# Kernel tuning notes

Hardware: AMD Instinct MI355X
Metric: run time of the kernel (lower is better)

## Reference

```python
import jax, jax.numpy as jnp
import numpy as np

N_NODES = 50000
N_EDGES = 500000
N_GRAPHS = 256
D_IN, D_H1, D_H2, D_H3, D_OUT = 768, 256, 128, 64, 2


def _glorot(key, shape):
    fan_in, fan_out = shape[1], shape[0]
    lim = float(np.sqrt(6.0 / (fan_in + fan_out)))
    return jax.random.uniform(key, shape, jnp.float32, -lim, lim)


def setup_inputs() -> dict:
    key = jax.random.key(0)
    ks = jax.random.split(key, 12)
    x = jax.random.normal(ks[0], (N_NODES, D_IN), jnp.float32)
    edge_index = jax.random.randint(ks[1], (2, N_EDGES), 0, N_NODES, jnp.int64)
    batch = jnp.sort(jax.random.randint(ks[2], (N_NODES,), 0, N_GRAPHS, jnp.int64))
    return {
        "x": x,
        "edge_index": edge_index,
        "batch": batch,
        # SAGEConv1: out = lin_l(mean_aggr) + lin_r(x); bias only on lin_l (PyG default)
        "W1_l": _glorot(ks[3], (D_H1, D_IN)),
        "b1_l": jnp.zeros((D_H1,), jnp.float32),
        "W1_r": _glorot(ks[4], (D_H1, D_IN)),
        # SAGEConv2
        "W2_l": _glorot(ks[5], (D_H2, D_H1)),
        "b2_l": jnp.zeros((D_H2,), jnp.float32),
        "W2_r": _glorot(ks[6], (D_H2, D_H1)),
        # MLP head
        "W3": _glorot(ks[7], (D_H3, D_H2)),
        "b3": jnp.zeros((D_H3,), jnp.float32),
        "W4": _glorot(ks[8], (D_OUT, D_H3)),
        "b4": jnp.zeros((D_OUT,), jnp.float32),
    }


def _sage_conv(x, src, dst, deg_inv, W_l, b_l, W_r):
    # mean aggregation of neighbor features: scatter-add then divide by in-degree
    aggr = jax.ops.segment_sum(x[src], dst, num_segments=N_NODES)  # [N, d]
    aggr = aggr * deg_inv[:, None]
    return aggr @ W_l.T + b_l + x @ W_r.T


def reference(x, edge_index, batch, W1_l, b1_l, W1_r, W2_l, b2_l, W2_r, W3, b3, W4, b4):
    src, dst = edge_index[0], edge_index[1]
    deg = jax.ops.segment_sum(jnp.ones((N_EDGES,), x.dtype), dst, num_segments=N_NODES)
    deg_inv = jnp.where(deg > 0, 1.0 / jnp.maximum(deg, 1.0), 0.0)

    h = jax.nn.relu(_sage_conv(x, src, dst, deg_inv, W1_l, b1_l, W1_r))
    h = jax.nn.relu(_sage_conv(h, src, dst, deg_inv, W2_l, b2_l, W2_r))

    # global_mean_pool over graph ids
    pooled = jax.ops.segment_sum(h, batch, num_segments=N_GRAPHS)  # [G, 128]
    cnt = jax.ops.segment_sum(jnp.ones((N_NODES,), h.dtype), batch, num_segments=N_GRAPHS)
    pooled = pooled / jnp.maximum(cnt, 1.0)[:, None]

    # dropout is identity in eval mode
    h = pooled @ W3.T + b3
    h = h @ W4.T + b4
    return jax.nn.softmax(h, axis=-1)
```

## Files before the change

### kernel.cpp

```cpp
#include <hip/hip_runtime.h>
#include <cstdint>
#include <cstddef>

#define N_NODES 50000
#define N_EDGES 500000
#define N_GRAPHS 256
#define D_IN 768
#define D_H1 256
#define D_H2 128

typedef __attribute__((ext_vector_type(8))) __bf16 bf16x8;
typedef __attribute__((ext_vector_type(4))) float f32x4;

__device__ __forceinline__ float bf2f(uint32_t u) {
    union { uint32_t i; float f; } v; v.i = u << 16; return v.f;
}
__device__ __forceinline__ uint32_t f2bf(float f) {
    union { float f; uint32_t i; } v; v.f = f;
    uint32_t u = v.i;
    return (u + 0x7FFFu + ((u >> 16) & 1u)) >> 16;
}

#define HIST4_BLKS 489
#define PACKA4_BLKS 4688
#define PACKW1_BLKS 192
#define PACKW2_BLKS 32
#define NCHUNK_A 4800000
__global__ __launch_bounds__(256) void k_pack_hist(
    const float* __restrict__ x, uint16_t* __restrict__ xp,
    const float* __restrict__ W1l, const float* __restrict__ W1r, uint16_t* __restrict__ W1p,
    const float* __restrict__ W2l, const float* __restrict__ W2r, uint16_t* __restrict__ W2p,
    const int* __restrict__ e_dst, int* __restrict__ deg)
{
    int b = blockIdx.x, t = threadIdx.x;
    if (b < HIST4_BLKS) {
        int base = b * 1024 + t;
        #pragma unroll
        for (int j = 0; j < 4; ++j) {
            int e = base + j * 256;
            if (e < N_EDGES) atomicAdd(&deg[e_dst[e]], 1);
        }
    } else if (b < HIST4_BLKS + PACKA4_BLKS) {
        int c0 = (b - HIST4_BLKS) * 1024 + t;
        float4 u[4], v[4];
        #pragma unroll
        for (int j = 0; j < 4; ++j) {
            int c = c0 + j * 256; if (c > NCHUNK_A - 1) c = NCHUNK_A - 1;
            int l = c & 63, tt = c >> 6;
            int kt = tt % 24, mt = tt / 24;
            const float* p = x + (size_t)(mt * 16 + (l & 15)) * 768 + kt * 32 + (l >> 4) * 8;
            u[j] = *(const float4*)p;
            v[j] = *(const float4*)(p + 4);
        }
        #pragma unroll
        for (int j = 0; j < 4; ++j) {
            int c = c0 + j * 256; if (c > NCHUNK_A - 1) c = NCHUNK_A - 1;
            uint4 o;
            o.x = f2bf(u[j].x) | (f2bf(u[j].y) << 16);
            o.y = f2bf(u[j].z) | (f2bf(u[j].w) << 16);
            o.z = f2bf(v[j].x) | (f2bf(v[j].y) << 16);
            o.w = f2bf(v[j].z) | (f2bf(v[j].w) << 16);
            *(uint4*)(xp + (size_t)c * 8) = o;
        }
    } else if (b < HIST4_BLKS + PACKA4_BLKS + PACKW1_BLKS) {
        int c = (b - HIST4_BLKS - PACKA4_BLKS) * 256 + t;
        int l = c & 63, tt = c >> 6;
        int kt = tt % 24, mt = tt / 24;
        int row = mt * 16 + (l & 15);
        const float* src = (row < 256) ? (W1l + (size_t)row * 768)
                                       : (W1r + (size_t)(row - 256) * 768);
        const float* p = src + kt * 32 + (l >> 4) * 8;
        float4 u = *(const float4*)p, v = *(const float4*)(p + 4);
        uint4 o;
        o.x = f2bf(u.x) | (f2bf(u.y) << 16);
        o.y = f2bf(u.z) | (f2bf(u.w) << 16);
        o.z = f2bf(v.x) | (f2bf(v.y) << 16);
        o.w = f2bf(v.z) | (f2bf(v.w) << 16);
        *(uint4*)(W1p + (size_t)c * 8) = o;
    } else {
        int c = (b - HIST4_BLKS - PACKA4_BLKS - PACKW1_BLKS) * 256 + t;
        int l = c & 63, tt = c >> 6;
        int kt = tt % 8, mt = tt / 8;
        int row = mt * 16 + (l & 15);
        const float* src = (row < 128) ? (W2l + (size_t)row * 256)
                                       : (W2r + (size_t)(row - 128) * 256);
        const float* p = src + kt * 32 + (l >> 4) * 8;
        float4 u = *(const float4*)p, v = *(const float4*)(p + 4);
        uint4 o;
        o.x = f2bf(u.x) | (f2bf(u.y) << 16);
        o.y = f2bf(u.z) | (f2bf(u.w) << 16);
        o.z = f2bf(v.x) | (f2bf(v.y) << 16);
        o.w = f2bf(v.z) | (f2bf(v.w) << 16);
        *(uint4*)(W2p + (size_t)c * 8) = o;
    }
}

__global__ __launch_bounds__(256) void k_scan(
    const int* __restrict__ deg, int* __restrict__ row_start, int* __restrict__ cursor,
    float* __restrict__ deg_inv, int* __restrict__ bsum, int n, int nb)
{
    __shared__ int buf[256];
    __shared__ int bbuf[256];
    int t = threadIdx.x, b = blockIdx.x, i = b * 256 + t;
    int v = (i < n) ? deg[i] : 0;
    buf[t] = v; __syncthreads();
    for (int off = 1; off < 256; off <<= 1) {
        int u = (t >= off) ? buf[t - off] : 0;
        __syncthreads(); buf[t] += u; __syncthreads();
    }
    if (t == 255) atomicExch(&bsum[b], buf[255] + 1);
    int w = 0;
    if (t < nb) {
        do { w = atomicAdd(&bsum[t], 0); } while (w == 0);
        w -= 1;
    }
    bbuf[t] = w; __syncthreads();
    for (int off = 1; off < 256; off <<= 1) {
        int u = (t >= off) ? bbuf[t - off] : 0;
        __syncthreads(); bbuf[t] += u; __syncthreads();
    }
    int base = (b > 0) ? bbuf[b - 1] : 0;
    if (i < n) {
        int rs = base + buf[t] - v;
        row_start[i] = rs;
        cursor[i] = rs;
        deg_inv[i] = (v > 0) ? (1.0f / (float)v) : 0.0f;
    }
    if (b == 0 && t == 0) row_start[n] = N_EDGES;
}

#define NSLAB 782
#define G1_GROUPS 98
#define G1_BLKS (G1_GROUPS * 16)
#define FILL_BLKS 1954
__global__ __launch_bounds__(256, 2) void k_gemm1_fill(
    const uint16_t* __restrict__ Ap, const uint16_t* __restrict__ Bp,
    uint16_t* __restrict__ Cl, uint16_t* __restrict__ Cr,
    const int* __restrict__ e_src, const int* __restrict__ e_dst,
    int* __restrict__ cursor, int* __restrict__ csr_src)
{
    int t = threadIdx.x;
    if (blockIdx.x >= G1_BLKS) {
        int e = (blockIdx.x - G1_BLKS) * 256 + t;
        if (e < N_EDGES) {
            int d = e_dst[e];
            int pos = atomicAdd(&cursor[d], 1);
            csr_src[pos] = e_src[e];
        }
        return;
    }
    const int i = blockIdx.x;
    const int pr = (i >> 4) * 8 + (i & 7);
    const int half = (i >> 3) & 1;
    if (pr >= NSLAB) return;
    const int KT = 24;
    const int wave = t >> 6, lane = t & 63;
    const int fr = lane & 15, fq = lane >> 4;
    const int bm = pr * 64;
    const int mtiles = (N_NODES + 15) >> 4;

    const bf16x8* ap[4];
    const bf16x8* bp[4];
    #pragma unroll
    for (int mi = 0; mi < 4; ++mi) {
        int mt = (bm >> 4) + mi;
        if (mt > mtiles - 1) mt = mtiles - 1;
        ap[mi] = (const bf16x8*)Ap + (size_t)mt * KT * 64 + lane;
    }
    #pragma unroll
    for (int ni = 0; ni < 4; ++ni) {
        int nt = half * 16 + wave * 4 + ni;
        bp[ni] = (const bf16x8*)Bp + (size_t)nt * KT * 64 + lane;
    }

    f32x4 acc[4][4] = {};
    bf16x8 a0[4], b0[4], a1[4], b1[4];

    auto lA = [&](int kt, bf16x8* d) {
        #pragma unroll
        for (int mi = 0; mi < 4; ++mi) d[mi] = ap[mi][kt * 64];
    };
    auto lB = [&](int kt, bf16x8* d) {
        #pragma unroll
        for (int ni = 0; ni < 4; ++ni) d[ni] = bp[ni][kt * 64];
    };
    auto step = [&](bf16x8* a, bf16x8* b) {
        #pragma unroll
        for (int mi = 0; mi < 4; ++mi)
            #pragma unroll
            for (int ni = 0; ni < 4; ++ni)
                acc[mi][ni] = __builtin_amdgcn_mfma_f32_16x16x32_bf16(
                    a[mi], b[ni], acc[mi][ni], 0, 0, 0);
    };

    lA(0, a0); lB(0, b0);
    for (int ks = 0; ks < KT; ks += 2) {
        lA(ks + 1, a1); lB(ks + 1, b1);
        step(a0, b0);
        if (ks + 2 < KT) { lA(ks + 2, a0); lB(ks + 2, b0); }
        step(a1, b1);
    }

    uint16_t* __restrict__ C = half ? Cr : Cl;
    #pragma unroll
    for (int mi = 0; mi < 4; ++mi) {
        #pragma unroll
        for (int r = 0; r < 4; ++r) {
            int row = bm + mi * 16 + fq * 4 + r;
            if (row >= N_NODES) continue;
            #pragma unroll
            for (int ni = 0; ni < 4; ++ni) {
                int col = wave * 64 + ni * 16 + fr;
                C[(size_t)row * 256 + col] = (uint16_t)f2bf(acc[mi][ni][r]);
            }
        }
    }
}

__global__ __launch_bounds__(256, 2) void k_mgemm(
    const uint16_t* __restrict__ Ap, const uint16_t* __restrict__ Bp,
    uint16_t* __restrict__ C, int M, int N, int KT)
{
    const int tid = threadIdx.x;
    const int wave = tid >> 6, lane = tid & 63;
    const int fr = lane & 15, fq = lane >> 4;
    const int bn = blockIdx.x * 256, bm = blockIdx.y * 128;
    const int wm = (wave >> 1) * 64, wn = (wave & 1) * 128;
    const int mtiles = (M + 15) >> 4;

    const bf16x8* ap[4];
    const bf16x8* bp[8];
    #pragma unroll
    for (int mi = 0; mi < 4; ++mi) {
        int mt = ((bm + wm) >> 4) + mi;
        if (mt > mtiles - 1) mt = mtiles - 1;
        ap[mi] = (const bf16x8*)Ap + (size_t)mt * KT * 64 + lane;
    }
    #pragma unroll
    for (int ni = 0; ni < 8; ++ni) {
        int nt = ((bn + wn) >> 4) + ni;
        bp[ni] = (const bf16x8*)Bp + (size_t)nt * KT * 64 + lane;
    }

    f32x4 acc[4][8] = {};
    bf16x8 a0[4], b0[8], a1[4], b1[8];

    auto lA = [&](int kt, bf16x8* d) {
        #pragma unroll
        for (int mi = 0; mi < 4; ++mi) d[mi] = ap[mi][kt * 64];
    };
    auto lB = [&](int kt, bf16x8* d) {
        #pragma unroll
        for (int ni = 0; ni < 8; ++ni) d[ni] = bp[ni][kt * 64];
    };
    auto step = [&](bf16x8* a, bf16x8* b) {
        #pragma unroll
        for (int mi = 0; mi < 4; ++mi)
            #pragma unroll
            for (int ni = 0; ni < 8; ++ni)
                acc[mi][ni] = __builtin_amdgcn_mfma_f32_16x16x32_bf16(
                    a[mi], b[ni], acc[mi][ni], 0, 0, 0);
    };

    lA(0, a0); lB(0, b0);
    for (int ks = 0; ks < KT; ks += 2) {
        lA(ks + 1, a1); lB(ks + 1, b1);
        step(a0, b0);
        if (ks + 2 < KT) { lA(ks + 2, a0); lB(ks + 2, b0); }
        step(a1, b1);
    }

    #pragma unroll
    for (int mi = 0; mi < 4; ++mi) {
        #pragma unroll
        for (int r = 0; r < 4; ++r) {
            int row = bm + wm + mi * 16 + fq * 4 + r;
            if (row >= M) continue;
            #pragma unroll
            for (int ni = 0; ni < 8; ++ni) {
                int col = bn + wn + ni * 16 + fr;
                C[(size_t)row * N + col] = (uint16_t)f2bf(acc[mi][ni][r]);
            }
        }
    }
}

__global__ __launch_bounds__(256) void k_agg1(
    const uint16_t* __restrict__ yl, const uint16_t* __restrict__ yr,
    const int* __restrict__ row_start, const int* __restrict__ csr,
    const float* __restrict__ deg_inv, const float* __restrict__ bias,
    uint16_t* __restrict__ h1p)
{
    int node = blockIdx.x * 8 + (threadIdx.x >> 5);
    if (node >= N_NODES) return;
    int c = threadIdx.x & 31;
    int s = row_start[node], e = row_start[node + 1];
    float a[8] = {};
    int p = s;
    auto accum = [&](uint4 t0) {
        a[0] += bf2f(t0.x & 0xFFFF); a[1] += bf2f(t0.x >> 16);
        a[2] += bf2f(t0.y & 0xFFFF); a[3] += bf2f(t0.y >> 16);
        a[4] += bf2f(t0.z & 0xFFFF); a[5] += bf2f(t0.z >> 16);
        a[6] += bf2f(t0.w & 0xFFFF); a[7] += bf2f(t0.w >> 16);
    };
    for (; p + 3 < e; p += 4) {
        uint4 t0 = *(const uint4*)(yl + (size_t)csr[p]     * 256 + c * 8);
        uint4 t1 = *(const uint4*)(yl + (size_t)csr[p + 1] * 256 + c * 8);
        uint4 t2 = *(const uint4*)(yl + (size_t)csr[p + 2] * 256 + c * 8);
        uint4 t3 = *(const uint4*)(yl + (size_t)csr[p + 3] * 256 + c * 8);
        accum(t0); accum(t1); accum(t2); accum(t3);
    }
    for (; p < e; ++p)
        accum(*(const uint4*)(yl + (size_t)csr[p] * 256 + c * 8));
    float w = deg_inv[node];
    uint4 tx = *(const uint4*)(yr + (size_t)node * 256 + c * 8);
    float4 b0 = *(const float4*)(bias + c * 8);
    float4 b1 = *(const float4*)(bias + c * 8 + 4);
    float v0 = fmaxf(a[0] * w + bf2f(tx.x & 0xFFFF) + b0.x, 0.f);
    float v1 = fmaxf(a[1] * w + bf2f(tx.x >> 16)    + b0.y, 0.f);
    float v2 = fmaxf(a[2] * w + bf2f(tx.y & 0xFFFF) + b0.z, 0.f);
    float v3 = fmaxf(a[3] * w + bf2f(tx.y >> 16)    + b0.w, 0.f);
    float v4 = fmaxf(a[4] * w + bf2f(tx.z & 0xFFFF) + b1.x, 0.f);
    float v5 = fmaxf(a[5] * w + bf2f(tx.z >> 16)    + b1.y, 0.f);
    float v6 = fmaxf(a[6] * w + bf2f(tx.w & 0xFFFF) + b1.z, 0.f);
    float v7 = fmaxf(a[7] * w + bf2f(tx.w >> 16)    + b1.w, 0.f);
    uint4 o;
    o.x = f2bf(v0) | (f2bf(v1) << 16);
    o.y = f2bf(v2) | (f2bf(v3) << 16);
    o.z = f2bf(v4) | (f2bf(v5) << 16);
    o.w = f2bf(v6) | (f2bf(v7) << 16);
    uint32_t addr = (((node >> 4) * 8 + (c >> 2)) * 64 + (c & 3) * 16 + (node & 15));
    *(uint4*)(h1p + (size_t)addr * 8) = o;
}

__global__ __launch_bounds__(256) void k_agg2(
    const uint16_t* __restrict__ y, const int* __restrict__ row_start,
    const int* __restrict__ csr, const float* __restrict__ deg_inv,
    const float* __restrict__ bias, float* __restrict__ out)
{
    int node = blockIdx.x * 4 + (threadIdx.x >> 6);
    if (node >= N_NODES) return;
    int lane = threadIdx.x & 63;
    int s = row_start[node], e = row_start[node + 1];
    float a0 = 0.f, a1 = 0.f;
    int p = s;
    for (; p + 3 < e; p += 4) {
        uint32_t t0 = *(const uint32_t*)(y + (size_t)csr[p]     * 256 + lane * 2);
        uint32_t t1 = *(const uint32_t*)(y + (size_t)csr[p + 1] * 256 + lane * 2);
        uint32_t t2 = *(const uint32_t*)(y + (size_t)csr[p + 2] * 256 + lane * 2);
        uint32_t t3 = *(const uint32_t*)(y + (size_t)csr[p + 3] * 256 + lane * 2);
        a0 += bf2f(t0 & 0xFFFF) + bf2f(t1 & 0xFFFF) + bf2f(t2 & 0xFFFF) + bf2f(t3 & 0xFFFF);
        a1 += bf2f(t0 >> 16)    + bf2f(t1 >> 16)    + bf2f(t2 >> 16)    + bf2f(t3 >> 16);
    }
    for (; p < e; ++p) {
        uint32_t t0 = *(const uint32_t*)(y + (size_t)csr[p] * 256 + lane * 2);
        a0 += bf2f(t0 & 0xFFFF);
        a1 += bf2f(t0 >> 16);
    }
    float w = deg_inv[node];
    uint32_t tx = *(const uint32_t*)(y + (size_t)node * 256 + 128 + lane * 2);
    float2 b = *(const float2*)(bias + lane * 2);
    float2 o;
    o.x = fmaxf(a0 * w + bf2f(tx & 0xFFFF) + b.x, 0.f);
    o.y = fmaxf(a1 * w + bf2f(tx >> 16)    + b.y, 0.f);
    *(float2*)(out + (size_t)node * 128 + lane * 2) = o;
}

__global__ void k_poolhead(const float* __restrict__ h2, const int* __restrict__ batch,
                           const float* __restrict__ W3, const float* __restrict__ b3,
                           const float* __restrict__ W4, const float* __restrict__ b4,
                           float* __restrict__ out)
{
    int g = blockIdx.x;
    __shared__ int s_lo, s_hi;
    __shared__ float p[128];
    __shared__ float hid[64];
    __shared__ float logit[2];
    int t = threadIdx.x;
    if (t == 0) {
        int lo = 0, hi = N_NODES;
        while (lo < hi) { int m = (lo + hi) >> 1; if (batch[m] < g) lo = m + 1; else hi = m; }
        s_lo = lo;
        int lo2 = lo, hi2 = N_NODES;
        while (lo2 < hi2) { int m = (lo2 + hi2) >> 1; if (batch[m] < g + 1) lo2 = m + 1; else hi2 = m; }
        s_hi = lo2;
    }
    __syncthreads();
    float sum = 0.f;
    for (int i = s_lo; i < s_hi; ++i) sum += h2[(size_t)i * D_H2 + t];
    int cnt = s_hi - s_lo;
    p[t] = sum / (float)(cnt > 0 ? cnt : 1);
    __syncthreads();
    if (t < 64) {
        float s = b3[t];
        #pragma unroll 4
        for (int k = 0; k < 128; ++k) s = fmaf(p[k], W3[t * 128 + k], s);
        hid[t] = s;
    }
    __syncthreads();
    if (t < 2) {
        float l = b4[t];
        for (int k = 0; k < 64; ++k) l = fmaf(hid[k], W4[t * 64 + k], l);
        logit[t] = l;
    }
    __syncthreads();
    if (t == 0) {
        float m = fmaxf(logit[0], logit[1]);
        float e0 = expf(logit[0] - m), e1 = expf(logit[1] - m);
        float inv = 1.0f / (e0 + e1);
        out[g * 2 + 0] = e0 * inv;
        out[g * 2 + 1] = e1 * inv;
    }
}

extern "C" void kernel_launch(void* const* d_in, const int* in_sizes, int n_in,
                              void* d_out, int out_size, void* d_ws, size_t ws_size,
                              hipStream_t stream)
{
    const float* x     = (const float*)d_in[0];
    const int*   ei    = (const int*)d_in[1];
    const int*   batch = (const int*)d_in[2];
    const float* W1l   = (const float*)d_in[3];
    const float* b1l   = (const float*)d_in[4];
    const float* W1r   = (const float*)d_in[5];
    const float* W2l   = (const float*)d_in[6];
    const float* b2l   = (const float*)d_in[7];
    const float* W2r   = (const float*)d_in[8];
    const float* W3    = (const float*)d_in[9];
    const float* b3    = (const float*)d_in[10];
    const float* W4    = (const float*)d_in[11];
    const float* b4    = (const float*)d_in[12];
    float* out = (float*)d_out;

    const int* e_src = ei;
    const int* e_dst = ei + N_EDGES;

    char* ws = (char*)d_ws;
    size_t off = 0;
    auto alloc = [&](size_t bytes) -> void* {
        void* p = ws + off;
        off = (off + bytes + 255) & ~(size_t)255;
        return p;
    };
    int*      deg       = (int*)alloc((size_t)(N_NODES + 256) * 4);
    int*      bsum      = deg + N_NODES;
    int*      row_start = (int*)alloc((size_t)(N_NODES + 1) * 4);
    int*      cursor    = (int*)alloc((size_t)N_NODES * 4);
    int*      csr_src   = (int*)alloc((size_t)N_EDGES * 4);
    float*    deg_inv   = (float*)alloc((size_t)N_NODES * 4);
    uint16_t* W1p       = (uint16_t*)alloc((size_t)512 * 768 * 2);
    uint16_t* W2p       = (uint16_t*)alloc((size_t)256 * 256 * 2);
    uint16_t* xp        = (uint16_t*)alloc((size_t)N_NODES * D_IN * 2);
    uint16_t* y1        = (uint16_t*)alloc((size_t)N_NODES * 512 * 2);
    uint16_t* h1p       = (uint16_t*)alloc((size_t)N_NODES * 256 * 2);

    uint16_t* y1l = y1;
    uint16_t* y1r = y1 + (size_t)N_NODES * 256;
    uint16_t* y2 = xp;
    float*    h2 = (float*)(xp + (size_t)N_NODES * 256);

    hipMemsetAsync(deg, 0, (size_t)(N_NODES + 256) * 4, stream);

    k_pack_hist<<<HIST4_BLKS + PACKA4_BLKS + PACKW1_BLKS + PACKW2_BLKS, 256, 0, stream>>>(
        x, xp, W1l, W1r, W1p, W2l, W2r, W2p, e_dst, deg);

    int nscan = (N_NODES + 255) / 256;
    k_scan<<<nscan, 256, 0, stream>>>(deg, row_start, cursor, deg_inv, bsum, N_NODES, nscan);

    k_gemm1_fill<<<G1_BLKS + FILL_BLKS, 256, 0, stream>>>(
        xp, W1p, y1l, y1r, e_src, e_dst, cursor, csr_src);
    k_agg1<<<(N_NODES + 7) / 8, 256, 0, stream>>>(y1l, y1r, row_start, csr_src, deg_inv, b1l, h1p);

    dim3 g2(1, (N_NODES + 127) / 128);
    k_mgemm<<<g2, 256, 0, stream>>>(h1p, W2p, y2, N_NODES, 256, 8);
    k_agg2<<<(N_NODES + 3) / 4, 256, 0, stream>>>(y2, row_start, csr_src, deg_inv, b2l, h2);

    k_poolhead<<<N_GRAPHS, 128, 0, stream>>>(h2, batch, W3, b3, W4, b4, out);
}
```

Measured before the change: 489.1 us.

## Fuse histogram, scan and CSR fill into one kernel with per-XCD counters

Merges the degree histogram, prefix scan and CSR fill into the packing kernel, synchronising through global atomic counters with spin-waits instead of separate launches. Degree counts are kept in per-XCD copies, chosen by reading the XCC id register, to cut cross-die atomic contention, and the scan writes per-XCD cursor offsets. The CSR fill moves out of the GEMM1 kernel, so GEMM1 runs alone. The design depends on all graph blocks being co-resident, since otherwise the spin-waits deadlock, and the memset grows eightfold.

```diff
diff --git a/kernel.cpp b/kernel.cpp
--- a/kernel.cpp
+++ b/kernel.cpp
@@ -8,6 +8,7 @@
 #define D_IN 768
 #define D_H1 256
 #define D_H2 128
+#define NXCD 8
 
 typedef __attribute__((ext_vector_type(8))) __bf16 bf16x8;
 typedef __attribute__((ext_vector_type(4))) float f32x4;
@@ -21,134 +22,171 @@
     return (u + 0x7FFFu + ((u >> 16) & 1u)) >> 16;
 }
 
-#define HIST4_BLKS 489
+#define GRAPH_BLKS 977
+#define SCAN_BLKS 196
 #define PACKA4_BLKS 4688
 #define PACKW1_BLKS 192
 #define PACKW2_BLKS 32
 #define NCHUNK_A 4800000
-__global__ __launch_bounds__(256) void k_pack_hist(
+#define XCC_GETREG_IMM 63508
+
+__global__ __launch_bounds__(256, 8) void k_graph_pack(
     const float* __restrict__ x, uint16_t* __restrict__ xp,
     const float* __restrict__ W1l, const float* __restrict__ W1r, uint16_t* __restrict__ W1p,
     const float* __restrict__ W2l, const float* __restrict__ W2r, uint16_t* __restrict__ W2p,
-    const int* __restrict__ e_dst, int* __restrict__ deg)
-{
+    const int* __restrict__ e_src, const int* __restrict__ e_dst,
+    int* __restrict__ degx,
+    int* __restrict__ row_start, float* __restrict__ deg_inv,
+    int* __restrict__ bsum, int* __restrict__ hist_done, int* __restrict__ scan_done,
+    int* __restrict__ csr_src)
+{
+    __shared__ int buf[256];
+    __shared__ int bbuf[256];
     int b = blockIdx.x, t = threadIdx.x;
-    if (b < HIST4_BLKS) {
-        int base = b * 1024 + t;
-        #pragma unroll
-        for (int j = 0; j < 4; ++j) {
-            int e = base + j * 256;
-            if (e < N_EDGES) atomicAdd(&deg[e_dst[e]], 1);
-        }
-    } else if (b < HIST4_BLKS + PACKA4_BLKS) {
-        int c0 = (b - HIST4_BLKS) * 1024 + t;
-        float4 u[4], v[4];
-        #pragma unroll
-        for (int j = 0; j < 4; ++j) {
-            int c = c0 + j * 256; if (c > NCHUNK_A - 1) c = NCHUNK_A - 1;
+
+    if (b >= GRAPH_BLKS) {
+        int b2 = b - GRAPH_BLKS;
+        if (b2 < PACKA4_BLKS) {
+            int c0 = b2 * 1024 + t;
+            float4 u[4], v[4];
+            #pragma unroll
+            for (int j = 0; j < 4; ++j) {
+                int c = c0 + j * 256; if (c > NCHUNK_A - 1) c = NCHUNK_A - 1;
+                int l = c & 63, tt = c >> 6;
+                int kt = tt % 24, mt = tt / 24;
+                const float* p = x + (size_t)(mt * 16 + (l & 15)) * 768 + kt * 32 + (l >> 4) * 8;
+                u[j] = *(const float4*)p;
+                v[j] = *(const float4*)(p + 4);
+            }
+            #pragma unroll
+            for (int j = 0; j < 4; ++j) {
+                int c = c0 + j * 256; if (c > NCHUNK_A - 1) c = NCHUNK_A - 1;
+                uint4 o;
+                o.x = f2bf(u[j].x) | (f2bf(u[j].y) << 16);
+                o.y = f2bf(u[j].z) | (f2bf(u[j].w) << 16);
+                o.z = f2bf(v[j].x) | (f2bf(v[j].y) << 16);
+                o.w = f2bf(v[j].z) | (f2bf(v[j].w) << 16);
+                *(uint4*)(xp + (size_t)c * 8) = o;
+            }
+        } else if (b2 < PACKA4_BLKS + PACKW1_BLKS) {
+            int c = (b2 - PACKA4_BLKS) * 256 + t;
             int l = c & 63, tt = c >> 6;
             int kt = tt % 24, mt = tt / 24;
-            const float* p = x + (size_t)(mt * 16 + (l & 15)) * 768 + kt * 32 + (l >> 4) * 8;
-            u[j] = *(const float4*)p;
-            v[j] = *(const float4*)(p + 4);
-        }
-        #pragma unroll
-        for (int j = 0; j < 4; ++j) {
-            int c = c0 + j * 256; if (c > NCHUNK_A - 1) c = NCHUNK_A - 1;
+            int row = mt * 16 + (l & 15);
+            const float* src = (row < 256) ? (W1l + (size_t)row * 768)
+                                           : (W1r + (size_t)(row - 256) * 768);
+            const float* p = src + kt * 32 + (l >> 4) * 8;
+            float4 u = *(const float4*)p, v = *(const float4*)(p + 4);
             uint4 o;
-            o.x = f2bf(u[j].x) | (f2bf(u[j].y) << 16);
-            o.y = f2bf(u[j].z) | (f2bf(u[j].w) << 16);
-            o.z = f2bf(v[j].x) | (f2bf(v[j].y) << 16);
-            o.w = f2bf(v[j].z) | (f2bf(v[j].w) << 16);
-            *(uint4*)(xp + (size_t)c * 8) = o;
-        }
-    } else if (b < HIST4_BLKS + PACKA4_BLKS + PACKW1_BLKS) {
-        int c = (b - HIST4_BLKS - PACKA4_BLKS) * 256 + t;
-        int l = c & 63, tt = c >> 6;
-        int kt = tt % 24, mt = tt / 24;
-        int row = mt * 16 + (l & 15);
-        const float* src = (row < 256) ? (W1l + (size_t)row * 768)
-                                       : (W1r + (size_t)(row - 256) * 768);
-        const float* p = src + kt * 32 + (l >> 4) * 8;
-        float4 u = *(const float4*)p, v = *(const float4*)(p + 4);
-        uint4 o;
-        o.x = f2bf(u.x) | (f2bf(u.y) << 16);
-        o.y = f2bf(u.z) | (f2bf(u.w) << 16);
-        o.z = f2bf(v.x) | (f2bf(v.y) << 16);
-        o.w = f2bf(v.z) | (f2bf(v.w) << 16);
-        *(uint4*)(W1p + (size_t)c * 8) = o;
-    } else {
-        int c = (b - HIST4_BLKS - PACKA4_BLKS - PACKW1_BLKS) * 256 + t;
-        int l = c & 63, tt = c >> 6;
-        int kt = tt % 8, mt = tt / 8;
-        int row = mt * 16 + (l & 15);
-        const float* src = (row < 128) ? (W2l + (size_t)row * 256)
-                                       : (W2r + (size_t)(row - 128) * 256);
-        const float* p = src + kt * 32 + (l >> 4) * 8;
-        float4 u = *(const float4*)p, v = *(const float4*)(p + 4);
-        uint4 o;
-        o.x = f2bf(u.x) | (f2bf(u.y) << 16);
-        o.y = f2bf(u.z) | (f2bf(u.w) << 16);
-        o.z = f2bf(v.x) | (f2bf(v.y) << 16);
-        o.w = f2bf(v.z) | (f2bf(v.w) << 16);
-        *(uint4*)(W2p + (size_t)c * 8) = o;
-    }
-}
-
-__global__ __launch_bounds__(256) void k_scan(
-    const int* __restrict__ deg, int* __restrict__ row_start, int* __restrict__ cursor,
-    float* __restrict__ deg_inv, int* __restrict__ bsum, int n, int nb)
-{
-    __shared__ int buf[256];
-    __shared__ int bbuf[256];
-    int t = threadIdx.x, b = blockIdx.x, i = b * 256 + t;
-    int v = (i < n) ? deg[i] : 0;
-    buf[t] = v; __syncthreads();
-    for (int off = 1; off < 256; off <<= 1) {
-        int u = (t >= off) ? buf[t - off] : 0;
-        __syncthreads(); buf[t] += u; __syncthreads();
-    }
-    if (t == 255) atomicExch(&bsum[b], buf[255] + 1);
-    int w = 0;
-    if (t < nb) {
-        do { w = atomicAdd(&bsum[t], 0); } while (w == 0);
-        w -= 1;
-    }
-    bbuf[t] = w; __syncthreads();
-    for (int off = 1; off < 256; off <<= 1) {
-        int u = (t >= off) ? bbuf[t - off] : 0;
-        __syncthreads(); bbuf[t] += u; __syncthreads();
-    }
-    int base = (b > 0) ? bbuf[b - 1] : 0;
-    if (i < n) {
-        int rs = base + buf[t] - v;
-        row_start[i] = rs;
-        cursor[i] = rs;
-        deg_inv[i] = (v > 0) ? (1.0f / (float)v) : 0.0f;
-    }
-    if (b == 0 && t == 0) row_start[n] = N_EDGES;
+            o.x = f2bf(u.x) | (f2bf(u.y) << 16);
+            o.y = f2bf(u.z) | (f2bf(u.w) << 16);
+            o.z = f2bf(v.x) | (f2bf(v.y) << 16);
+            o.w = f2bf(v.z) | (f2bf(v.w) << 16);
+            *(uint4*)(W1p + (size_t)c * 8) = o;
+        } else {
+            int c = (b2 - PACKA4_BLKS - PACKW1_BLKS) * 256 + t;
+            int l = c & 63, tt = c >> 6;
+            int kt = tt % 8, mt = tt / 8;
+            int row = mt * 16 + (l & 15);
+            const float* src = (row < 128) ? (W2l + (size_t)row * 256)
+                                           : (W2r + (size_t)(row - 128) * 256);
+            const float* p = src + kt * 32 + (l >> 4) * 8;
+            float4 u = *(const float4*)p, v = *(const float4*)(p + 4);
+            uint4 o;
+            o.x = f2bf(u.x) | (f2bf(u.y) << 16);
+            o.y = f2bf(u.z) | (f2bf(u.w) << 16);
+            o.z = f2bf(v.x) | (f2bf(v.y) << 16);
+            o.w = f2bf(v.z) | (f2bf(v.w) << 16);
+            *(uint4*)(W2p + (size_t)c * 8) = o;
+        }
+        return;
+    }
+
+    int gb = b;
+    uint32_t xcc = __builtin_amdgcn_s_getreg(XCC_GETREG_IMM) & (NXCD - 1);
+    int* mycnt = degx + (size_t)xcc * N_NODES;
+    int e0 = gb * 512 + t;
+    int e1 = e0 + 256;
+    int d0 = (e0 < N_EDGES) ? e_dst[e0] : -1;
+    int d1 = (e1 < N_EDGES) ? e_dst[e1] : -1;
+
+    if (d0 >= 0) atomicAdd(&mycnt[d0], 1);
+    if (d1 >= 0) atomicAdd(&mycnt[d1], 1);
+    __threadfence();
+    __syncthreads();
+    if (t == 0)
+        __hip_atomic_fetch_add(hist_done, 1, __ATOMIC_RELEASE, __HIP_MEMORY_SCOPE_AGENT);
+
+    if (gb < SCAN_BLKS) {
+        if (t == 0) {
+            while (__hip_atomic_load(hist_done, __ATOMIC_ACQUIRE,
+                                     __HIP_MEMORY_SCOPE_AGENT) < GRAPH_BLKS)
+                __builtin_amdgcn_s_sleep(8);
+        }
+        __syncthreads();
+        int i = gb * 256 + t;
+        int dxl[8]; int v = 0;
+        #pragma unroll
+        for (int xx = 0; xx < NXCD; ++xx) {
+            int dv = 0;
+            if (i < N_NODES)
+                dv = __hip_atomic_load(&degx[(size_t)xx * N_NODES + i],
+                                       __ATOMIC_RELAXED, __HIP_MEMORY_SCOPE_AGENT);
+            dxl[xx] = dv; v += dv;
+        }
+        buf[t] = v; __syncthreads();
+        for (int off = 1; off < 256; off <<= 1) {
+            int u = (t >= off) ? buf[t - off] : 0;
+            __syncthreads(); buf[t] += u; __syncthreads();
+        }
+        if (t == 255) atomicExch(&bsum[gb], buf[255] + 1);
+        int w = 0;
+        if (t < SCAN_BLKS) {
+            do { w = atomicAdd(&bsum[t], 0); } while (w == 0);
+            w -= 1;
+        }
+        bbuf[t] = w; __syncthreads();
+        for (int off = 1; off < 256; off <<= 1) {
+            int u = (t >= off) ? bbuf[t - off] : 0;
+            __syncthreads(); bbuf[t] += u; __syncthreads();
+        }
+        int base = (gb > 0) ? bbuf[gb - 1] : 0;
+        if (i < N_NODES) {
+            int rs = base + buf[t] - v;
+            row_start[i] = rs;
+            deg_inv[i] = (v > 0) ? (1.0f / (float)v) : 0.0f;
+            int acc = rs;
+            #pragma unroll
+            for (int xx = 0; xx < NXCD; ++xx) {
+                degx[(size_t)xx * N_NODES + i] = acc;
+                acc += dxl[xx];
+            }
+        }
+        if (gb == 0 && t == 0) row_start[N_NODES] = N_EDGES;
+        __threadfence();
+        __syncthreads();
+        if (t == 0)
+            __hip_atomic_fetch_add(scan_done, 1, __ATOMIC_RELEASE, __HIP_MEMORY_SCOPE_AGENT);
+    }
+
+    if (t == 0) {
+        while (__hip_atomic_load(scan_done, __ATOMIC_ACQUIRE,
+                                 __HIP_MEMORY_SCOPE_AGENT) < SCAN_BLKS)
+            __builtin_amdgcn_s_sleep(8);
+    }
+    __syncthreads();
+    if (d0 >= 0) { int pos = atomicAdd(&mycnt[d0], 1); csr_src[pos] = e_src[e0]; }
+    if (d1 >= 0) { int pos = atomicAdd(&mycnt[d1], 1); csr_src[pos] = e_src[e1]; }
 }
 
 #define NSLAB 782
 #define G1_GROUPS 98
 #define G1_BLKS (G1_GROUPS * 16)
-#define FILL_BLKS 1954
-__global__ __launch_bounds__(256, 2) void k_gemm1_fill(
+__global__ __launch_bounds__(256, 2) void k_gemm1(
     const uint16_t* __restrict__ Ap, const uint16_t* __restrict__ Bp,
-    uint16_t* __restrict__ Cl, uint16_t* __restrict__ Cr,
-    const int* __restrict__ e_src, const int* __restrict__ e_dst,
-    int* __restrict__ cursor, int* __restrict__ csr_src)
+    uint16_t* __restrict__ Cl, uint16_t* __restrict__ Cr)
 {
     int t = threadIdx.x;
-    if (blockIdx.x >= G1_BLKS) {
-        int e = (blockIdx.x - G1_BLKS) * 256 + t;
-        if (e < N_EDGES) {
-            int d = e_dst[e];
-            int pos = atomicAdd(&cursor[d], 1);
-            csr_src[pos] = e_src[e];
-        }
-        return;
-    }
     const int i = blockIdx.x;
     const int pr = (i >> 4) * 8 + (i & 7);
     const int half = (i >> 3) & 1;
@@ -442,10 +480,11 @@
         off = (off + bytes + 255) & ~(size_t)255;
         return p;
     };
-    int*      deg       = (int*)alloc((size_t)(N_NODES + 256) * 4);
-    int*      bsum      = deg + N_NODES;
+    int*      degx      = (int*)alloc((size_t)(NXCD * N_NODES + 256 + 64) * 4);
+    int*      bsum      = degx + NXCD * N_NODES;
+    int*      hist_done = bsum + 256;
+    int*      scan_done = hist_done + 1;
     int*      row_start = (int*)alloc((size_t)(N_NODES + 1) * 4);
-    int*      cursor    = (int*)alloc((size_t)N_NODES * 4);
     int*      csr_src   = (int*)alloc((size_t)N_EDGES * 4);
     float*    deg_inv   = (float*)alloc((size_t)N_NODES * 4);
     uint16_t* W1p       = (uint16_t*)alloc((size_t)512 * 768 * 2);
@@ -459,16 +498,13 @@
     uint16_t* y2 = xp;
     float*    h2 = (float*)(xp + (size_t)N_NODES * 256);
 
-    hipMemsetAsync(deg, 0, (size_t)(N_NODES + 256) * 4, stream);
-
-    k_pack_hist<<<HIST4_BLKS + PACKA4_BLKS + PACKW1_BLKS + PACKW2_BLKS, 256, 0, stream>>>(
-        x, xp, W1l, W1r, W1p, W2l, W2r, W2p, e_dst, deg);
-
-    int nscan = (N_NODES + 255) / 256;
-    k_scan<<<nscan, 256, 0, stream>>>(deg, row_start, cursor, deg_inv, bsum, N_NODES, nscan);
-
-    k_gemm1_fill<<<G1_BLKS + FILL_BLKS, 256, 0, stream>>>(
-        xp, W1p, y1l, y1r, e_src, e_dst, cursor, csr_src);
+    hipMemsetAsync(degx, 0, (size_t)(NXCD * N_NODES + 256 + 64) * 4, stream);
+
+    k_graph_pack<<<GRAPH_BLKS + PACKA4_BLKS + PACKW1_BLKS + PACKW2_BLKS, 256, 0, stream>>>(
+        x, xp, W1l, W1r, W1p, W2l, W2r, W2p, e_src, e_dst,
+        degx, row_start, deg_inv, bsum, hist_done, scan_done, csr_src);
+
+    k_gemm1<<<G1_BLKS, 256, 0, stream>>>(xp, W1p, y1l, y1r);
     k_agg1<<<(N_NODES + 7) / 8, 256, 0, stream>>>(y1l, y1r, row_start, csr_src, deg_inv, b1l, h1p);
 
     dim3 g2(1, (N_NODES + 127) / 128);
```

Result: slower. 716.1 us (+46.4%).

## Privatize degree histogram and CSR fill cursors per XCD

Applied to the files above, without the earlier changes.

Splits the in-degree histogram and the CSR fill cursors into 8 copies, one per XCD (chosen by block index mod 8), so atomics from different dies do not contend on the same cache lines across the chip. The scan sums the 8 copies and writes per-copy starting offsets. The fill kernel then uses the matching copy, with 4 edges per thread. The trade-off is a larger memset and extra reads and writes in the scan, and it assumes blocks are assigned to XCDs round-robin.

```diff
diff --git a/kernel.cpp b/kernel.cpp
--- a/kernel.cpp
+++ b/kernel.cpp
@@ -8,6 +8,7 @@
 #define D_IN 768
 #define D_H1 256
 #define D_H2 128
+#define NXCD 8
 
 typedef __attribute__((ext_vector_type(8))) __bf16 bf16x8;
 typedef __attribute__((ext_vector_type(4))) float f32x4;
@@ -30,15 +31,16 @@
     const float* __restrict__ x, uint16_t* __restrict__ xp,
     const float* __restrict__ W1l, const float* __restrict__ W1r, uint16_t* __restrict__ W1p,
     const float* __restrict__ W2l, const float* __restrict__ W2r, uint16_t* __restrict__ W2p,
-    const int* __restrict__ e_dst, int* __restrict__ deg)
+    const int* __restrict__ e_dst, int* __restrict__ degx)
 {
     int b = blockIdx.x, t = threadIdx.x;
     if (b < HIST4_BLKS) {
+        int* mycnt = degx + (size_t)(b & 7) * N_NODES;
         int base = b * 1024 + t;
         #pragma unroll
         for (int j = 0; j < 4; ++j) {
             int e = base + j * 256;
-            if (e < N_EDGES) atomicAdd(&deg[e_dst[e]], 1);
+            if (e < N_EDGES) atomicAdd(&mycnt[e_dst[e]], 1);
         }
     } else if (b < HIST4_BLKS + PACKA4_BLKS) {
         int c0 = (b - HIST4_BLKS) * 1024 + t;
@@ -96,13 +98,18 @@
 }
 
 __global__ __launch_bounds__(256) void k_scan(
-    const int* __restrict__ deg, int* __restrict__ row_start, int* __restrict__ cursor,
-    float* __restrict__ deg_inv, int* __restrict__ bsum, int n, int nb)
+    int* __restrict__ degx, int* __restrict__ row_start,
+    float* __restrict__ deg_inv, int* __restrict__ bsum, int nb)
 {
     __shared__ int buf[256];
     __shared__ int bbuf[256];
     int t = threadIdx.x, b = blockIdx.x, i = b * 256 + t;
-    int v = (i < n) ? deg[i] : 0;
+    int dxl[NXCD]; int v = 0;
+    #pragma unroll
+    for (int xx = 0; xx < NXCD; ++xx) {
+        int dv = (i < N_NODES) ? degx[(size_t)xx * N_NODES + i] : 0;
+        dxl[xx] = dv; v += dv;
+    }
     buf[t] = v; __syncthreads();
     for (int off = 1; off < 256; off <<= 1) {
         int u = (t >= off) ? buf[t - off] : 0;
@@ -120,32 +127,43 @@
         __syncthreads(); bbuf[t] += u; __syncthreads();
     }
     int base = (b > 0) ? bbuf[b - 1] : 0;
-    if (i < n) {
+    if (i < N_NODES) {
         int rs = base + buf[t] - v;
         row_start[i] = rs;
-        cursor[i] = rs;
         deg_inv[i] = (v > 0) ? (1.0f / (float)v) : 0.0f;
-    }
-    if (b == 0 && t == 0) row_start[n] = N_EDGES;
+        int acc = rs;
+        #pragma unroll
+        for (int xx = 0; xx < NXCD; ++xx) {
+            degx[(size_t)xx * N_NODES + i] = acc;
+            acc += dxl[xx];
+        }
+    }
+    if (b == 0 && t == 0) row_start[N_NODES] = N_EDGES;
 }
 
 #define NSLAB 782
 #define G1_GROUPS 98
 #define G1_BLKS (G1_GROUPS * 16)
-#define FILL_BLKS 1954
+#define FILL4_BLKS 489
 __global__ __launch_bounds__(256, 2) void k_gemm1_fill(
     const uint16_t* __restrict__ Ap, const uint16_t* __restrict__ Bp,
     uint16_t* __restrict__ Cl, uint16_t* __restrict__ Cr,
     const int* __restrict__ e_src, const int* __restrict__ e_dst,
-    int* __restrict__ cursor, int* __restrict__ csr_src)
+    int* __restrict__ degx, int* __restrict__ csr_src)
 {
     int t = threadIdx.x;
     if (blockIdx.x >= G1_BLKS) {
-        int e = (blockIdx.x - G1_BLKS) * 256 + t;
-        if (e < N_EDGES) {
-            int d = e_dst[e];
-            int pos = atomicAdd(&cursor[d], 1);
-            csr_src[pos] = e_src[e];
+        int j = blockIdx.x - G1_BLKS;
+        int* mycur = degx + (size_t)(j & 7) * N_NODES;
+        int base = j * 1024 + t;
+        #pragma unroll
+        for (int k = 0; k < 4; ++k) {
+            int e = base + k * 256;
+            if (e < N_EDGES) {
+                int d = e_dst[e];
+                int pos = atomicAdd(&mycur[d], 1);
+                csr_src[pos] = e_src[e];
+            }
         }
         return;
     }
@@ -442,10 +460,9 @@
         off = (off + bytes + 255) & ~(size_t)255;
         return p;
     };
-    int*      deg       = (int*)alloc((size_t)(N_NODES + 256) * 4);
-    int*      bsum      = deg + N_NODES;
+    int*      degx      = (int*)alloc((size_t)(NXCD * N_NODES + 256) * 4);
+    int*      bsum      = degx + NXCD * N_NODES;
     int*      row_start = (int*)alloc((size_t)(N_NODES + 1) * 4);
-    int*      cursor    = (int*)alloc((size_t)N_NODES * 4);
     int*      csr_src   = (int*)alloc((size_t)N_EDGES * 4);
     float*    deg_inv   = (float*)alloc((size_t)N_NODES * 4);
     uint16_t* W1p       = (uint16_t*)alloc((size_t)512 * 768 * 2);
@@ -459,16 +476,16 @@
     uint16_t* y2 = xp;
     float*    h2 = (float*)(xp + (size_t)N_NODES * 256);
 
-    hipMemsetAsync(deg, 0, (size_t)(N_NODES + 256) * 4, stream);
+    hipMemsetAsync(degx, 0, (size_t)(NXCD * N_NODES + 256) * 4, stream);
 
     k_pack_hist<<<HIST4_BLKS + PACKA4_BLKS + PACKW1_BLKS + PACKW2_BLKS, 256, 0, stream>>>(
-        x, xp, W1l, W1r, W1p, W2l, W2r, W2p, e_dst, deg);
+        x, xp, W1l, W1r, W1p, W2l, W2r, W2p, e_dst, degx);
 
     int nscan = (N_NODES + 255) / 256;
-    k_scan<<<nscan, 256, 0, stream>>>(deg, row_start, cursor, deg_inv, bsum, N_NODES, nscan);
-
-    k_gemm1_fill<<<G1_BLKS + FILL_BLKS, 256, 0, stream>>>(
-        xp, W1p, y1l, y1r, e_src, e_dst, cursor, csr_src);
+    k_scan<<<nscan, 256, 0, stream>>>(degx, row_start, deg_inv, bsum, nscan);
+
+    k_gemm1_fill<<<G1_BLKS + FILL4_BLKS, 256, 0, stream>>>(
+        xp, W1p, y1l, y1r, e_src, e_dst, degx, csr_src);
     k_agg1<<<(N_NODES + 7) / 8, 256, 0, stream>>>(y1l, y1r, row_start, csr_src, deg_inv, b1l, h1p);
 
     dim3 g2(1, (N_NODES + 127) / 128);
```

After: 497.2 us. Within noise of the previous version (+1.7%).
